# Kernel optimization log

Hardware: AMD Instinct MI355X
Metric: run time of the kernel (lower is better)

## Reference

```python
import jax, jax.numpy as jnp
import numpy as np

NEG_SLOPE = 0.2  # PyG GATConv default negative_slope


def gat_layer(x, src, dst, W, b, att_src, att_dst, heads, concat):
    """PyG-style GATConv (eval mode, self-loops already in src/dst).
    x: [N, F_in], W: [F_in, heads*hd], att_*: [heads, hd], b: [out_dim].
    """
    N = x.shape[0]
    hd = W.shape[1] // heads
    h = (x @ W).reshape(N, heads, hd)                      # [N, H, D]
    a_s = jnp.einsum('nhd,hd->nh', h, att_src)             # [N, H]
    a_d = jnp.einsum('nhd,hd->nh', h, att_dst)             # [N, H]
    e = jax.nn.leaky_relu(a_s[src] + a_d[dst], NEG_SLOPE)  # [E, H]
    # segment softmax over edges sharing a destination node
    m = jax.ops.segment_max(e, dst, num_segments=N)        # [N, H]
    m = jnp.where(jnp.isfinite(m), m, 0.0)
    ex = jnp.exp(e - m[dst])
    den = jax.ops.segment_sum(ex, dst, num_segments=N)     # [N, H]
    alpha = ex / (den[dst] + 1e-16)                        # [E, H]
    out = jax.ops.segment_sum(h[src] * alpha[:, :, None], dst, num_segments=N)  # [N,H,D]
    out = out.reshape(N, heads * hd) if concat else out.mean(axis=1)
    return out + b


def setup_inputs() -> dict:
    key = jax.random.key(0)
    ks = jax.random.split(key, 16)
    N, E, F_IN, HID, H, C = 100000, 1600000, 256, 128, 8, 6
    HD = HID // H
    s = 0.1
    return {
        'x': jax.random.normal(ks[0], (N, F_IN), jnp.float32),
        'edge_index': jax.random.randint(ks[1], (2, E), 0, N, jnp.int64),
        'W1': jax.random.normal(ks[2], (F_IN, HID), jnp.float32) * s,
        'b1': jnp.zeros((HID,), jnp.float32),
        'att_src1': jax.random.normal(ks[3], (H, HD), jnp.float32) * s,
        'att_dst1': jax.random.normal(ks[4], (H, HD), jnp.float32) * s,
        'W2': jax.random.normal(ks[5], (HID, HID), jnp.float32) * s,
        'b2': jnp.zeros((HID,), jnp.float32),
        'att_src2': jax.random.normal(ks[6], (H, HD), jnp.float32) * s,
        'att_dst2': jax.random.normal(ks[7], (H, HD), jnp.float32) * s,
        'W3': jax.random.normal(ks[8], (HID, C), jnp.float32) * s,
        'b3': jnp.zeros((C,), jnp.float32),
        'att_src3': jax.random.normal(ks[9], (1, C), jnp.float32) * s,
        'att_dst3': jax.random.normal(ks[10], (1, C), jnp.float32) * s,
    }


def reference(x, edge_index, W1, b1, att_src1, att_dst1, W2, b2, att_src2, att_dst2,
              W3, b3, att_src3, att_dst3):
    N = x.shape[0]
    loops = jnp.arange(N, dtype=edge_index.dtype)
    src = jnp.concatenate([edge_index[0], loops])  # add self-loops (PyG default)
    dst = jnp.concatenate([edge_index[1], loops])
    h = jax.nn.elu(gat_layer(x, src, dst, W1, b1, att_src1, att_dst1, 8, True))
    h = jax.nn.elu(gat_layer(h, src, dst, W2, b2, att_src2, att_dst2, 8, True))
    return gat_layer(h, src, dst, W3, b3, att_src3, att_dst3, 1, False)
```

## Files before the change

### kernel.cpp

```cpp
#include <hip/hip_runtime.h>
#include <hip/hip_bf16.h>
#include <cstdint>

typedef unsigned short u16;
typedef __attribute__((ext_vector_type(8))) short bf16x8;
typedef __attribute__((ext_vector_type(4))) float f32x4;

#define CAP 48

__device__ __forceinline__ float b2f(u16 u){
  union { unsigned int i; float f; } v; v.i = ((unsigned int)u) << 16; return v.f;
}
__device__ __forceinline__ u16 f2b(float f){
  union { float f; unsigned int i; } v; v.f = f;
  unsigned int x = v.i;
  x += 0x7fff + ((x >> 16) & 1);
  return (u16)(x >> 16);
}
__device__ __forceinline__ float lrelu(float x){ return x > 0.f ? x : 0.2f * x; }

__global__ void k_flags(const u16* __restrict__ xr, const int* __restrict__ ei,
                        int* __restrict__ flags){
  __shared__ float smax[256];
  int t = threadIdx.x;
  float v = fabsf(b2f(xr[t * 2]));
  if (!isfinite(v)) v = 1e30f;
  smax[t] = v;
  __syncthreads();
  for (int off = 128; off > 0; off >>= 1){
    if (t < off) smax[t] = fmaxf(smax[t], smax[t + off]);
    __syncthreads();
  }
  if (t == 0){
    flags[0] = (smax[0] > 1e4f) ? 1 : 0;
    int allz = 1;
    for (int i = 1; i < 32; i += 2) if (ei[i] != 0) allz = 0;
    flags[1] = allz;
    flags[2] = 0;
    flags[3] = 0;
  }
}

#define PW_W1 0
#define PW_B1 32768
#define PW_AS1 32896
#define PW_AD1 33024
#define PW_W2 33152
#define PW_B2 49536
#define PW_AS2 49664
#define PW_AD2 49792
#define PW_W3 49920
#define PW_B3 50688
#define PW_AS3 50694
#define PW_AD3 50700
#define PW_TOTAL 50706

__global__ void k_cvt_params(const void* p0, const void* p1, const void* p2, const void* p3,
                             const void* p4, const void* p5, const void* p6, const void* p7,
                             const void* p8, const void* p9, const void* p10, const void* p11,
                             u16* __restrict__ pw, const int* __restrict__ flags){
  int i = blockIdx.x * blockDim.x + threadIdx.x;
  if (i >= PW_TOTAL) return;
  const int sizes[12] = {32768,128,128,128,16384,128,128,128,768,6,6,6};
  const void* ptrs[12] = {p0,p1,p2,p3,p4,p5,p6,p7,p8,p9,p10,p11};
  int off = 0, seg = 0, loc = 0;
  for (int s = 0; s < 12; s++){
    if (i < off + sizes[s]){ seg = s; loc = i - off; break; }
    off += sizes[s];
  }
  float v = flags[0] ? ((const float*)ptrs[seg])[loc] : b2f(((const u16*)ptrs[seg])[loc]);
  pw[i] = f2b(v);
}

__global__ void k_transpose(const u16* __restrict__ src, u16* __restrict__ dst, int R, int C){
  int i = blockIdx.x * blockDim.x + threadIdx.x;
  if (i >= R * C) return;
  int r = i / C, c = i - r * C;
  dst[(size_t)c * R + r] = src[i];
}

__device__ __forceinline__ int eread(const int* __restrict__ ei, int idx, int is64){
  return ei[is64 ? (idx << 1) : idx];
}

__global__ __launch_bounds__(256) void k_scatter_gemm1(const int* __restrict__ ei, int E,
                                                       int* __restrict__ cnt, int* __restrict__ ebuf,
                                                       const int* __restrict__ flags, int SB,
                                                       const void* __restrict__ Xv,
                                                       const u16* __restrict__ WT,
                                                       u16* __restrict__ Ho, int N){
  if ((int)blockIdx.x < SB){
    int is64 = flags[1];
    for (int i = blockIdx.x * blockDim.x + threadIdx.x; i < E; i += SB * blockDim.x){
      int s = eread(ei, i, is64);
      int d = eread(ei, E + i, is64);
      int pos = atomicAdd(&cnt[d], 1);
      if (pos < CAP) ebuf[d * CAP + pos] = s;
    }
    return;
  }
  constexpr int K = 256;
  int bid = (int)blockIdx.x - SB;
  int gwave = (bid * 256 + (int)threadIdx.x) >> 6;
  int lane = threadIdx.x & 63;
  int n0 = gwave * 32;
  if (n0 >= N) return;
  int quad = lane >> 4, l15 = lane & 15;
  int r0 = n0 + l15;        if (r0 >= N) r0 = N - 1;
  int r1 = n0 + 16 + l15;   if (r1 >= N) r1 = N - 1;
  const u16* wbase = WT + (size_t)l15 * K + quad * 8;
  f32x4 acc[2][8] = {};
  if (flags[0]){
    const float* x0p = (const float*)Xv + (size_t)r0 * K + quad * 8;
    const float* x1p = (const float*)Xv + (size_t)r1 * K + quad * 8;
    for (int k0 = 0; k0 < K; k0 += 32){
      float4 v00 = *(const float4*)(x0p + k0);
      float4 v01 = *(const float4*)(x0p + k0 + 4);
      float4 v10 = *(const float4*)(x1p + k0);
      float4 v11 = *(const float4*)(x1p + k0 + 4);
      bf16x8 a0, a1;
      a0[0]=(short)f2b(v00.x); a0[1]=(short)f2b(v00.y); a0[2]=(short)f2b(v00.z); a0[3]=(short)f2b(v00.w);
      a0[4]=(short)f2b(v01.x); a0[5]=(short)f2b(v01.y); a0[6]=(short)f2b(v01.z); a0[7]=(short)f2b(v01.w);
      a1[0]=(short)f2b(v10.x); a1[1]=(short)f2b(v10.y); a1[2]=(short)f2b(v10.z); a1[3]=(short)f2b(v10.w);
      a1[4]=(short)f2b(v11.x); a1[5]=(short)f2b(v11.y); a1[6]=(short)f2b(v11.z); a1[7]=(short)f2b(v11.w);
      #pragma unroll
      for (int c = 0; c < 8; c++){
        bf16x8 b = *(const bf16x8*)(wbase + (size_t)c * 16 * K + k0);
        acc[0][c] = __builtin_amdgcn_mfma_f32_16x16x32_bf16(a0, b, acc[0][c], 0, 0, 0);
        acc[1][c] = __builtin_amdgcn_mfma_f32_16x16x32_bf16(a1, b, acc[1][c], 0, 0, 0);
      }
    }
  } else {
    const u16* x0p = (const u16*)Xv + (size_t)r0 * K + quad * 8;
    const u16* x1p = (const u16*)Xv + (size_t)r1 * K + quad * 8;
    for (int k0 = 0; k0 < K; k0 += 32){
      bf16x8 a0 = *(const bf16x8*)(x0p + k0);
      bf16x8 a1 = *(const bf16x8*)(x1p + k0);
      #pragma unroll
      for (int c = 0; c < 8; c++){
        bf16x8 b = *(const bf16x8*)(wbase + (size_t)c * 16 * K + k0);
        acc[0][c] = __builtin_amdgcn_mfma_f32_16x16x32_bf16(a0, b, acc[0][c], 0, 0, 0);
        acc[1][c] = __builtin_amdgcn_mfma_f32_16x16x32_bf16(a1, b, acc[1][c], 0, 0, 0);
      }
    }
  }
  #pragma unroll
  for (int t = 0; t < 2; t++){
    #pragma unroll
    for (int c = 0; c < 8; c++){
      #pragma unroll
      for (int r = 0; r < 4; r++){
        int row = n0 + t * 16 + quad * 4 + r;
        if (row < N) Ho[(size_t)row * 128 + c * 16 + l15] = f2b(acc[t][c][r]);
      }
    }
  }
}

template<int K>
__global__ __launch_bounds__(256) void k_gemm_mfma(const void* __restrict__ Xv,
                                                   const u16* __restrict__ WT,
                                                   u16* __restrict__ Ho, int N,
                                                   const int* __restrict__ flags){
  int gwave = (blockIdx.x * blockDim.x + threadIdx.x) >> 6;
  int lane = threadIdx.x & 63;
  int n0 = gwave * 32;
  if (n0 >= N) return;
  int quad = lane >> 4, l15 = lane & 15;
  int r0 = n0 + l15;        if (r0 >= N) r0 = N - 1;
  int r1 = n0 + 16 + l15;   if (r1 >= N) r1 = N - 1;
  const u16* wbase = WT + (size_t)l15 * K + quad * 8;
  f32x4 acc[2][8] = {};
  const u16* x0p = (const u16*)Xv + (size_t)r0 * K + quad * 8;
  const u16* x1p = (const u16*)Xv + (size_t)r1 * K + quad * 8;
  for (int k0 = 0; k0 < K; k0 += 32){
    bf16x8 a0 = *(const bf16x8*)(x0p + k0);
    bf16x8 a1 = *(const bf16x8*)(x1p + k0);
    #pragma unroll
    for (int c = 0; c < 8; c++){
      bf16x8 b = *(const bf16x8*)(wbase + (size_t)c * 16 * K + k0);
      acc[0][c] = __builtin_amdgcn_mfma_f32_16x16x32_bf16(a0, b, acc[0][c], 0, 0, 0);
      acc[1][c] = __builtin_amdgcn_mfma_f32_16x16x32_bf16(a1, b, acc[1][c], 0, 0, 0);
    }
  }
  #pragma unroll
  for (int t = 0; t < 2; t++){
    #pragma unroll
    for (int c = 0; c < 8; c++){
      #pragma unroll
      for (int r = 0; r < 4; r++){
        int row = n0 + t * 16 + quad * 4 + r;
        if (row < N) Ho[(size_t)row * 128 + c * 16 + l15] = f2b(acc[t][c][r]);
      }
    }
  }
}

__global__ __launch_bounds__(256) void k_gemm3(const u16* __restrict__ X, const u16* __restrict__ W,
                                               u16* __restrict__ Ho, int N){
  __shared__ float sW[128 * 6];
  for (int i = threadIdx.x; i < 128 * 6; i += blockDim.x) sW[i] = b2f(W[i]);
  __syncthreads();
  int n = blockIdx.x * blockDim.x + threadIdx.x;
  if (n >= N) return;
  const u16* xr = X + (size_t)n * 128;
  float acc[6] = {0, 0, 0, 0, 0, 0};
  #pragma unroll 8
  for (int k = 0; k < 128; k += 2){
    unsigned int xp = *(const unsigned int*)(xr + k);
    float x0 = b2f((u16)(xp & 0xffff));
    float x1 = b2f((u16)(xp >> 16));
    const float* w0 = sW + k * 6;
    #pragma unroll
    for (int j = 0; j < 6; j++) acc[j] += x0 * w0[j] + x1 * w0[6 + j];
  }
  u16* out = Ho + (size_t)n * 6;
  #pragma unroll
  for (int j = 0; j < 6; j++) out[j] = f2b(acc[j]);
}

template<int H, int D>
__global__ __launch_bounds__(256) void k_att(const u16* __restrict__ Hbuf,
                                             const u16* __restrict__ AS, const u16* __restrict__ AD,
                                             float* __restrict__ as_o, float* __restrict__ ad_o, int N){
  int t = blockIdx.x * blockDim.x + threadIdx.x;
  if (t >= N * H) return;
  int n = t / H, h = t - n * H;
  const u16* hp = Hbuf + (size_t)n * (H * D) + h * D;
  float s1 = 0, s2 = 0;
  #pragma unroll
  for (int d = 0; d < D; d++){
    float v = b2f(hp[d]);
    s1 += v * b2f(AS[h * D + d]);
    s2 += v * b2f(AD[h * D + d]);
  }
  as_o[t] = s1; ad_o[t] = s2;
}

template<int H, int D, int EPI>
__global__ __launch_bounds__(256) void k_agg(const u16* __restrict__ Hbuf, const float* __restrict__ as,
                                             const float* __restrict__ ad,
                                             const int* __restrict__ cnt, const int* __restrict__ ebuf,
                                             const u16* __restrict__ bias, void* __restrict__ outv,
                                             const int* __restrict__ flags, int N){
  constexpr int DP = D / 2;
  constexpr int LPN = H * DP;
  constexpr int NPW = 64 / LPN;
  int wave = (blockIdx.x * blockDim.x + threadIdx.x) >> 6;
  int lane = threadIdx.x & 63;
  int sub = lane / LPN;
  int rem = lane - sub * LPN;
  int n = wave * NPW + sub;
  if (sub >= NPW || n >= N) return;
  int head = rem / DP, dp = rem - head * DP;
  int nh = n * H + head;
  float adi = ad[nh];
  size_t hoff = (size_t)head * D + 2 * dp;
  float w = __expf(lrelu(as[nh] + adi));
  unsigned int hp = *(const unsigned int*)(Hbuf + (size_t)n * (H * D) + hoff);
  float den = w;
  float a0 = w * b2f((u16)(hp & 0xffff));
  float a1 = w * b2f((u16)(hp >> 16));
  int deg = cnt[n]; if (deg > CAP) deg = CAP;
  const int* row = ebuf + n * CAP;
  int j = 0;
  for (; j + 4 <= deg; j += 4){
    int s0 = row[j], s1 = row[j + 1], s2 = row[j + 2], s3 = row[j + 3];
    float v0 = as[s0 * H + head];
    float v1 = as[s1 * H + head];
    float v2 = as[s2 * H + head];
    float v3 = as[s3 * H + head];
    unsigned int q0 = *(const unsigned int*)(Hbuf + (size_t)s0 * (H * D) + hoff);
    unsigned int q1 = *(const unsigned int*)(Hbuf + (size_t)s1 * (H * D) + hoff);
    unsigned int q2 = *(const unsigned int*)(Hbuf + (size_t)s2 * (H * D) + hoff);
    unsigned int q3 = *(const unsigned int*)(Hbuf + (size_t)s3 * (H * D) + hoff);
    float w0 = __expf(lrelu(v0 + adi));
    float w1 = __expf(lrelu(v1 + adi));
    float w2 = __expf(lrelu(v2 + adi));
    float w3 = __expf(lrelu(v3 + adi));
    den += (w0 + w1) + (w2 + w3);
    a0 += w0 * b2f((u16)(q0 & 0xffff)) + w1 * b2f((u16)(q1 & 0xffff))
        + w2 * b2f((u16)(q2 & 0xffff)) + w3 * b2f((u16)(q3 & 0xffff));
    a1 += w0 * b2f((u16)(q0 >> 16)) + w1 * b2f((u16)(q1 >> 16))
        + w2 * b2f((u16)(q2 >> 16)) + w3 * b2f((u16)(q3 >> 16));
  }
  for (; j < deg; j++){
    int s = row[j];
    float w2 = __expf(lrelu(as[s * H + head] + adi));
    unsigned int hq = *(const unsigned int*)(Hbuf + (size_t)s * (H * D) + hoff);
    den += w2;
    a0 += w2 * b2f((u16)(hq & 0xffff));
    a1 += w2 * b2f((u16)(hq >> 16));
  }
  float inv = 1.f / (den + 1e-16f);
  a0 *= inv; a1 *= inv;
  int jidx = head * D + 2 * dp;
  a0 += b2f(bias[jidx]);
  a1 += b2f(bias[jidx + 1]);
  if (EPI == 0){
    a0 = a0 > 0.f ? a0 : expm1f(a0);
    a1 = a1 > 0.f ? a1 : expm1f(a1);
    unsigned int packed = (unsigned int)f2b(a0) | ((unsigned int)f2b(a1) << 16);
    *(unsigned int*)((u16*)outv + (size_t)n * (H * D) + jidx) = packed;
  } else {
    if (flags[0]){
      float2* o = (float2*)((float*)outv + (size_t)n * (H * D) + jidx);
      *o = make_float2(a0, a1);
    } else {
      unsigned int packed = (unsigned int)f2b(a0) | ((unsigned int)f2b(a1) << 16);
      *(unsigned int*)((u16*)outv + (size_t)n * (H * D) + jidx) = packed;
    }
  }
}

extern "C" void kernel_launch(void* const* d_in, const int* in_sizes, int n_in,
                              void* d_out, int out_size, void* d_ws, size_t ws_size,
                              hipStream_t stream){
  const void* x   = d_in[0];
  const int*  ei  = (const int*)d_in[1];

  const int N = in_sizes[0] / 256;
  const int E = in_sizes[1] / 2;

  char* p = (char*)d_ws;
  auto alloc = [&](size_t bytes){ void* q = (void*)p; p += (bytes + 255) & ~(size_t)255; return q; };
  int*   flags  = (int*)alloc(256);
  int*   cnt    = (int*)alloc((size_t)N * 4);
  int*   ebuf   = (int*)alloc((size_t)N * CAP * 4);
  u16*   hbuf   = (u16*)alloc((size_t)N * 128 * 2);
  float* asb    = (float*)alloc((size_t)N * 8 * 4);
  float* adb    = (float*)alloc((size_t)N * 8 * 4);
  u16*   x2     = (u16*)alloc((size_t)N * 128 * 2);
  u16*   x3     = (u16*)alloc((size_t)N * 128 * 2);
  u16*   pw     = (u16*)alloc((size_t)PW_TOTAL * 2);
  u16*   wt1    = (u16*)alloc((size_t)128 * 256 * 2);
  u16*   wt2    = (u16*)alloc((size_t)128 * 128 * 2);

  const int tb = 256;

  k_flags<<<1, 256, 0, stream>>>((const u16*)x, ei, flags);
  k_cvt_params<<<(PW_TOTAL + tb - 1) / tb, tb, 0, stream>>>(
      d_in[2], d_in[3], d_in[4], d_in[5], d_in[6], d_in[7],
      d_in[8], d_in[9], d_in[10], d_in[11], d_in[12], d_in[13], pw, flags);
  k_transpose<<<(32768 + tb - 1) / tb, tb, 0, stream>>>(pw + PW_W1, wt1, 256, 128);
  k_transpose<<<(16384 + tb - 1) / tb, tb, 0, stream>>>(pw + PW_W2, wt2, 128, 128);
  hipMemsetAsync(cnt, 0, (size_t)N * 4, stream);

  int gemm_blocks = (N + 127) / 128;
  const int SB = 1024;

  k_scatter_gemm1<<<SB + gemm_blocks, tb, 0, stream>>>(ei, E, cnt, ebuf, flags, SB,
                                                       x, wt1, hbuf, N);
  k_att<8, 16><<<(N * 8 + tb - 1) / tb, tb, 0, stream>>>(hbuf, pw + PW_AS1, pw + PW_AD1, asb, adb, N);
  k_agg<8, 16, 0><<<((size_t)N * 64 + tb - 1) / tb, tb, 0, stream>>>(hbuf, asb, adb, cnt, ebuf, pw + PW_B1, x2, flags, N);

  k_gemm_mfma<128><<<gemm_blocks, tb, 0, stream>>>(x2, wt2, hbuf, N, flags + 2);
  k_att<8, 16><<<(N * 8 + tb - 1) / tb, tb, 0, stream>>>(hbuf, pw + PW_AS2, pw + PW_AD2, asb, adb, N);
  k_agg<8, 16, 0><<<((size_t)N * 64 + tb - 1) / tb, tb, 0, stream>>>(hbuf, asb, adb, cnt, ebuf, pw + PW_B2, x3, flags, N);

  k_gemm3<<<(N + tb - 1) / tb, tb, 0, stream>>>(x3, pw + PW_W3, hbuf, N);
  k_att<1, 6><<<(N + tb - 1) / tb, tb, 0, stream>>>(hbuf, pw + PW_AS3, pw + PW_AD3, asb, adb, N);
  int waves3 = (N + 20) / 21;
  k_agg<1, 6, 1><<<((size_t)waves3 * 64 + tb - 1) / tb, tb, 0, stream>>>(hbuf, asb, adb, cnt, ebuf, pw + PW_B3, d_out, flags, N);
}
```

Baseline: 545.5 us.

## Replace global atomic edge scatter with two-pass bucketed partition and LDS CSR build

The per-edge global atomicAdd scatter into per-node slots is replaced by a two-pass partition. Edges are first histogrammed per block into 128-node buckets in shared memory, then written as packed (src,dst-local) words into per-bucket buffers. A second kernel builds each bucket's per-node edge lists in LDS and writes them out contiguously. That kernel also fuses in the layer-1 attention-coefficient computation. The aim is to cut global atomic contention and scattered writes, at the cost of an extra pass over the edges, a fixed bucket capacity (BCAP) that can drop edges if a bucket overflows, and a src<<7 packing that limits node ids.

```diff
diff --git a/kernel.cpp b/kernel.cpp
--- a/kernel.cpp
+++ b/kernel.cpp
@@ -7,6 +7,10 @@
 typedef __attribute__((ext_vector_type(4))) float f32x4;
 
 #define CAP 48
+#define NPB 128
+#define BCAP 2560
+#define SA 128
+#define MAXBUK 1024
 
 __device__ __forceinline__ float b2f(u16 u){
   union { unsigned int i; float f; } v; v.i = ((unsigned int)u) << 16; return v.f;
@@ -83,24 +87,44 @@
   return ei[is64 ? (idx << 1) : idx];
 }
 
-__global__ __launch_bounds__(256) void k_scatter_gemm1(const int* __restrict__ ei, int E,
-                                                       int* __restrict__ cnt, int* __restrict__ ebuf,
-                                                       const int* __restrict__ flags, int SB,
-                                                       const void* __restrict__ Xv,
-                                                       const u16* __restrict__ WT,
-                                                       u16* __restrict__ Ho, int N){
-  if ((int)blockIdx.x < SB){
+__global__ __launch_bounds__(256) void k_part_gemm1(const int* __restrict__ ei, int E,
+                                                    unsigned* __restrict__ bbuf,
+                                                    int* __restrict__ gcnt, int NBUK,
+                                                    const int* __restrict__ flags,
+                                                    const void* __restrict__ Xv,
+                                                    const u16* __restrict__ WT,
+                                                    u16* __restrict__ Ho, int N){
+  if ((int)blockIdx.x < SA){
+    __shared__ int hist[MAXBUK];
+    __shared__ int sbase[MAXBUK];
+    int tid = threadIdx.x;
     int is64 = flags[1];
-    for (int i = blockIdx.x * blockDim.x + threadIdx.x; i < E; i += SB * blockDim.x){
+    int e0 = (int)((long long)blockIdx.x * E / SA);
+    int e1 = (int)((long long)((int)blockIdx.x + 1) * E / SA);
+    for (int i = tid; i < NBUK; i += 256) hist[i] = 0;
+    __syncthreads();
+    for (int i = e0 + tid; i < e1; i += 256){
+      int d = eread(ei, E + i, is64);
+      atomicAdd(&hist[d >> 7], 1);
+    }
+    __syncthreads();
+    for (int i = tid; i < NBUK; i += 256){
+      sbase[i] = atomicAdd(&gcnt[i], hist[i]);
+      hist[i] = 0;
+    }
+    __syncthreads();
+    for (int i = e0 + tid; i < e1; i += 256){
       int s = eread(ei, i, is64);
       int d = eread(ei, E + i, is64);
-      int pos = atomicAdd(&cnt[d], 1);
-      if (pos < CAP) ebuf[d * CAP + pos] = s;
+      int b = d >> 7;
+      int r = sbase[b] + atomicAdd(&hist[b], 1);
+      if (r < BCAP)
+        bbuf[(size_t)b * BCAP + r] = ((unsigned)s << 7) | (unsigned)(d & (NPB - 1));
     }
     return;
   }
   constexpr int K = 256;
-  int bid = (int)blockIdx.x - SB;
+  int bid = (int)blockIdx.x - SA;
   int gwave = (bid * 256 + (int)threadIdx.x) >> 6;
   int lane = threadIdx.x & 63;
   int n0 = gwave * 32;
@@ -155,6 +179,50 @@
       }
     }
   }
+}
+
+__global__ __launch_bounds__(256) void k_build_att(const unsigned* __restrict__ bbuf,
+                                                   const int* __restrict__ gcnt,
+                                                   int* __restrict__ cnt, int* __restrict__ ebuf,
+                                                   int NBUK, int N,
+                                                   const u16* __restrict__ Hbuf,
+                                                   const u16* __restrict__ AS,
+                                                   const u16* __restrict__ AD,
+                                                   float* __restrict__ as_o,
+                                                   float* __restrict__ ad_o){
+  if ((int)blockIdx.x < NBUK){
+    __shared__ int lcnt[NPB];
+    __shared__ int lrow[NPB * CAP];
+    int b = blockIdx.x, tid = threadIdx.x;
+    for (int i = tid; i < NPB; i += 256) lcnt[i] = 0;
+    __syncthreads();
+    int m = gcnt[b]; if (m > BCAP) m = BCAP;
+    const unsigned* bp = bbuf + (size_t)b * BCAP;
+    for (int i = tid; i < m; i += 256){
+      unsigned e = bp[i];
+      int dl = e & (NPB - 1);
+      int p = atomicAdd(&lcnt[dl], 1);
+      if (p < CAP) lrow[dl * CAP + p] = (int)(e >> 7);
+    }
+    __syncthreads();
+    int n0 = b * NPB;
+    int lim = N - n0; if (lim > NPB) lim = NPB;
+    for (int i = tid; i < lim * CAP; i += 256) ebuf[(size_t)n0 * CAP + i] = lrow[i];
+    for (int i = tid; i < lim; i += 256) cnt[n0 + i] = lcnt[i];
+    return;
+  }
+  int t = ((int)blockIdx.x - NBUK) * 256 + (int)threadIdx.x;
+  if (t >= N * 8) return;
+  int n = t >> 3, h = t & 7;
+  const u16* hp = Hbuf + (size_t)n * 128 + h * 16;
+  float s1 = 0, s2 = 0;
+  #pragma unroll
+  for (int d = 0; d < 16; d++){
+    float v = b2f(hp[d]);
+    s1 += v * b2f(AS[h * 16 + d]);
+    s2 += v * b2f(AD[h * 16 + d]);
+  }
+  as_o[t] = s1; ad_o[t] = s2;
 }
 
 template<int K>
@@ -321,20 +389,23 @@
 
   const int N = in_sizes[0] / 256;
   const int E = in_sizes[1] / 2;
+  const int NBUK = (N + NPB - 1) / NPB;
 
   char* p = (char*)d_ws;
   auto alloc = [&](size_t bytes){ void* q = (void*)p; p += (bytes + 255) & ~(size_t)255; return q; };
-  int*   flags  = (int*)alloc(256);
-  int*   cnt    = (int*)alloc((size_t)N * 4);
-  int*   ebuf   = (int*)alloc((size_t)N * CAP * 4);
-  u16*   hbuf   = (u16*)alloc((size_t)N * 128 * 2);
-  float* asb    = (float*)alloc((size_t)N * 8 * 4);
-  float* adb    = (float*)alloc((size_t)N * 8 * 4);
-  u16*   x2     = (u16*)alloc((size_t)N * 128 * 2);
-  u16*   x3     = (u16*)alloc((size_t)N * 128 * 2);
-  u16*   pw     = (u16*)alloc((size_t)PW_TOTAL * 2);
-  u16*   wt1    = (u16*)alloc((size_t)128 * 256 * 2);
-  u16*   wt2    = (u16*)alloc((size_t)128 * 128 * 2);
+  int*      flags  = (int*)alloc(256);
+  int*      cnt    = (int*)alloc((size_t)N * 4);
+  int*      ebuf   = (int*)alloc((size_t)N * CAP * 4);
+  u16*      hbuf   = (u16*)alloc((size_t)N * 128 * 2);
+  float*    asb    = (float*)alloc((size_t)N * 8 * 4);
+  float*    adb    = (float*)alloc((size_t)N * 8 * 4);
+  u16*      x2     = (u16*)alloc((size_t)N * 128 * 2);
+  u16*      x3     = (u16*)alloc((size_t)N * 128 * 2);
+  u16*      pw     = (u16*)alloc((size_t)PW_TOTAL * 2);
+  u16*      wt1    = (u16*)alloc((size_t)128 * 256 * 2);
+  u16*      wt2    = (u16*)alloc((size_t)128 * 128 * 2);
+  unsigned* bbuf   = (unsigned*)alloc((size_t)NBUK * BCAP * 4);
+  int*      gcnt   = (int*)alloc((size_t)NBUK * 4);
 
   const int tb = 256;
 
@@ -344,18 +415,19 @@
       d_in[8], d_in[9], d_in[10], d_in[11], d_in[12], d_in[13], pw, flags);
   k_transpose<<<(32768 + tb - 1) / tb, tb, 0, stream>>>(pw + PW_W1, wt1, 256, 128);
   k_transpose<<<(16384 + tb - 1) / tb, tb, 0, stream>>>(pw + PW_W2, wt2, 128, 128);
-  hipMemsetAsync(cnt, 0, (size_t)N * 4, stream);
+  hipMemsetAsync(gcnt, 0, (size_t)NBUK * 4, stream);
 
   int gemm_blocks = (N + 127) / 128;
-  const int SB = 1024;
-
-  k_scatter_gemm1<<<SB + gemm_blocks, tb, 0, stream>>>(ei, E, cnt, ebuf, flags, SB,
-                                                       x, wt1, hbuf, N);
-  k_att<8, 16><<<(N * 8 + tb - 1) / tb, tb, 0, stream>>>(hbuf, pw + PW_AS1, pw + PW_AD1, asb, adb, N);
+  int att_blocks  = (N * 8 + tb - 1) / tb;
+
+  k_part_gemm1<<<SA + gemm_blocks, tb, 0, stream>>>(ei, E, bbuf, gcnt, NBUK, flags,
+                                                    x, wt1, hbuf, N);
+  k_build_att<<<NBUK + att_blocks, tb, 0, stream>>>(bbuf, gcnt, cnt, ebuf, NBUK, N,
+                                                    hbuf, pw + PW_AS1, pw + PW_AD1, asb, adb);
   k_agg<8, 16, 0><<<((size_t)N * 64 + tb - 1) / tb, tb, 0, stream>>>(hbuf, asb, adb, cnt, ebuf, pw + PW_B1, x2, flags, N);
 
   k_gemm_mfma<128><<<gemm_blocks, tb, 0, stream>>>(x2, wt2, hbuf, N, flags + 2);
-  k_att<8, 16><<<(N * 8 + tb - 1) / tb, tb, 0, stream>>>(hbuf, pw + PW_AS2, pw + PW_AD2, asb, adb, N);
+  k_att<8, 16><<<att_blocks, tb, 0, stream>>>(hbuf, pw + PW_AS2, pw + PW_AD2, asb, adb, N);
   k_agg<8, 16, 0><<<((size_t)N * 64 + tb - 1) / tb, tb, 0, stream>>>(hbuf, asb, adb, cnt, ebuf, pw + PW_B2, x3, flags, N);
 
   k_gemm3<<<(N + tb - 1) / tb, tb, 0, stream>>>(x3, pw + PW_W3, hbuf, N);
```

Result: faster. 512.9 us (-6.0%).
